# Kernel tuning notes

Hardware: AMD Instinct MI355X
Metric: run time of the kernel (lower is better)

The kernel has to match this reference:

```python
import jax, jax.numpy as jnp
import numpy as np
import math

HIDDEN = 2048
NUM_HEADS = 16
HEAD_DIM = HIDDEN // NUM_HEADS  # 128
B, T = 2, 2048
MAX_POS = 4096
ROPE_BASE = 10000.0


def _rope_cache(dim, max_pos, base):
    inv_freq = 1.0 / (base ** (jnp.arange(0, dim, 2, dtype=jnp.float32) / dim))
    t = jnp.arange(max_pos, dtype=jnp.float32)
    freqs = jnp.einsum('i,j->ij', t, inv_freq)        # [max_pos, dim/2]
    emb = jnp.concatenate([freqs, freqs], axis=-1)     # [max_pos, dim]
    return jnp.cos(emb), jnp.sin(emb)


def setup_inputs() -> dict:
    key = jax.random.key(0)
    ks = jax.random.split(key, 5)
    hidden_states = jax.random.normal(ks[0], (B, T, HIDDEN), dtype=jnp.float32)
    # additive causal mask, large negative (not -inf) for numerical safety
    causal = jnp.triu(jnp.full((T, T), -1e9, dtype=jnp.float32), k=1)
    attention_mask = causal[None, None, :, :]          # [1,1,T,T]
    position_ids = jnp.arange(T, dtype=jnp.int64)
    s = 1.0 / math.sqrt(HIDDEN)
    Wq = jax.random.normal(ks[1], (HIDDEN, HIDDEN), dtype=jnp.float32) * s
    Wk = jax.random.normal(ks[2], (HIDDEN, HIDDEN), dtype=jnp.float32) * s
    Wv = jax.random.normal(ks[3], (HIDDEN, HIDDEN), dtype=jnp.float32) * s
    Wo = jax.random.normal(ks[4], (HIDDEN, HIDDEN), dtype=jnp.float32) * s
    cos_cached, sin_cached = _rope_cache(HEAD_DIM, MAX_POS, ROPE_BASE)
    return {
        'hidden_states': hidden_states,
        'attention_mask': attention_mask,
        'position_ids': position_ids,
        'Wq': Wq, 'Wk': Wk, 'Wv': Wv, 'Wo': Wo,
        'cos_cached': cos_cached, 'sin_cached': sin_cached,
    }


def _apply_rope(x, cos, sin):
    # x: [B, T, nh, hd]; cos/sin: [T, 1, hd] (broadcast over heads)
    x1 = x[..., 0::2]
    x2 = x[..., 1::2]
    x_rot = jnp.stack([-x2, x1], axis=-1).reshape(x.shape)  # interleaved rotate
    return x * cos + x_rot * sin


def reference(hidden_states, attention_mask, position_ids, Wq, Wk, Wv, Wo,
              cos_cached, sin_cached):
    Bs, Ts, H = hidden_states.shape
    nh, hd = NUM_HEADS, HEAD_DIM
    q = (hidden_states @ Wq.T).reshape(Bs, Ts, nh, hd)
    k = (hidden_states @ Wk.T).reshape(Bs, Ts, nh, hd)
    v = (hidden_states @ Wv.T).reshape(Bs, Ts, nh, hd)
    cos = cos_cached[position_ids][:, None, :]  # [T,1,hd]
    sin = sin_cached[position_ids][:, None, :]
    q = _apply_rope(q, cos, sin)
    k = _apply_rope(k, cos, sin)
    # [B, nh, T, hd]
    q = q.transpose(0, 2, 1, 3)
    k = k.transpose(0, 2, 1, 3)
    v = v.transpose(0, 2, 1, 3)
    scores = jnp.einsum('bhqd,bhkd->bhqk', q, k) / math.sqrt(hd)
    scores = scores + attention_mask
    attn = jax.nn.softmax(scores, axis=-1)
    out = jnp.einsum('bhqk,bhkd->bhqd', attn, v)
    out = out.transpose(0, 2, 1, 3).reshape(Bs, Ts, H)
    return out @ Wo.T
```

## Files before the change

kernel.cpp:

```cpp
#include <hip/hip_runtime.h>
#include <cstdint>


typedef __bf16 v8bf __attribute__((ext_vector_type(8)));
typedef float  v4f  __attribute__((ext_vector_type(4)));
typedef float  f32x16 __attribute__((ext_vector_type(16)));

__device__ __forceinline__ uint16_t f2bf(float f) {
  union { float f; uint32_t u; } v; v.f = f;
  uint32_t u = v.u;
  return (uint16_t)((u + 0x7FFFu + ((u >> 16) & 1u)) >> 16);
}

__device__ __forceinline__ uint32_t cvtpk(float lo, float hi) {
  uint32_t w;
  asm("v_cvt_pk_bf16_f32 %0, %1, %2" : "=v"(w) : "v"(lo), "v"(hi));
  return w;
}

__device__ __forceinline__ void gload16(const void* g, void* l) {
  __builtin_amdgcn_global_load_lds(
      (const __attribute__((address_space(1))) void*)g,
      (__attribute__((address_space(3))) void*)l, 16, 0, 0);
}

__global__ void cvt_all_kernel(const float* __restrict__ s0, uint16_t* d0,
                               const float* __restrict__ s1, uint16_t* d1,
                               const float* __restrict__ s2, uint16_t* d2,
                               const float* __restrict__ s3, uint16_t* d3,
                               const float* __restrict__ s4, uint16_t* d4) {
  const float* src; uint16_t* dst; int n4;
  switch (blockIdx.y) {
    case 0: src = s0; dst = d0; n4 = 2097152; break;
    case 1: src = s1; dst = d1; n4 = 1048576; break;
    case 2: src = s2; dst = d2; n4 = 1048576; break;
    case 3: src = s3; dst = d3; n4 = 1048576; break;
    default: src = s4; dst = d4; n4 = 1048576; break;
  }
  int i = blockIdx.x * blockDim.x + threadIdx.x;
  int stride = gridDim.x * blockDim.x;
  for (; i < n4; i += stride) {
    float4 v = reinterpret_cast<const float4*>(src)[i];
    ushort4 o;
    o.x = f2bf(v.x); o.y = f2bf(v.y); o.z = f2bf(v.z); o.w = f2bf(v.w);
    reinterpret_cast<ushort4*>(dst)[i] = o;
  }
}

__device__ __forceinline__ void gemm256_mainloop(
    const uint16_t* __restrict__ A, const uint16_t* __restrict__ Bt,
    int m0, int n0, uint16_t* As, uint16_t* Bs, v4f acc[4][4]) {
  const int tid  = threadIdx.x;
  const int lane = tid & 63, w = tid >> 6;
  const int wm = w >> 1, wn = w & 1;
  const int lrow = lane & 15, lhi = lane >> 4;

  auto stageA = [&](int buf, int k0, int i) {
    int c = i * 512 + tid;
    int row = c >> 3, seg = c & 7;
    int sseg = seg ^ (row & 7);
    gload16(A + (size_t)(m0 + row) * 2048 + k0 + sseg * 8,
            As + buf * 16384 + c * 8);
  };
  auto stageB = [&](int buf, int k0, int i) {
    int c = i * 512 + tid;
    int row = c >> 3, seg = c & 7;
    int sseg = seg ^ (row & 7);
    gload16(Bt + (size_t)(n0 + row) * 2048 + k0 + sseg * 8,
            Bs + buf * 8192 + c * 8);
  };

#pragma unroll
  for (int i = 0; i < 4; ++i) stageA(0, 0, i);
#pragma unroll
  for (int i = 0; i < 2; ++i) stageB(0, 0, i);
#pragma unroll
  for (int i = 0; i < 4; ++i) stageA(1, 64, i);
#pragma unroll
  for (int i = 0; i < 2; ++i) stageB(1, 64, i);
  asm volatile("s_waitcnt vmcnt(6)" ::: "memory");
  __builtin_amdgcn_s_barrier();
  __builtin_amdgcn_sched_barrier(0);

  for (int t = 0; t < 32; ++t) {
    const int cb = t % 3;
    const int sb = (t + 2) % 3;
    const int sk = (t + 2) * 64;
    const uint16_t* Ac = As + cb * 16384;
    const uint16_t* Bc = Bs + cb * 8192;
    const bool do_stage = (t + 2) < 32;
#pragma unroll
    for (int ks = 0; ks < 2; ++ks) {
      v8bf af[4], bfv[4];
#pragma unroll
      for (int mf = 0; mf < 4; ++mf) {
        const int ar = wm * 64 + mf * 16 + lrow;
        const int seg = (ks * 4 + lhi) ^ (ar & 7);
        af[mf] = *reinterpret_cast<const v8bf*>(Ac + ar * 64 + seg * 8);
      }
#pragma unroll
      for (int nf = 0; nf < 4; ++nf) {
        const int br = wn * 64 + nf * 16 + lrow;
        const int seg = (ks * 4 + lhi) ^ (br & 7);
        bfv[nf] = *reinterpret_cast<const v8bf*>(Bc + br * 64 + seg * 8);
      }
      if (do_stage) {
        if (ks == 0) { stageA(sb, sk, 0); stageA(sb, sk, 1); stageB(sb, sk, 0); }
        else         { stageA(sb, sk, 2); stageA(sb, sk, 3); stageB(sb, sk, 1); }
      }
      if (ks == 1) {
        if (t < 30) asm volatile("s_waitcnt vmcnt(6)" ::: "memory");
        else        asm volatile("s_waitcnt vmcnt(0)" ::: "memory");
      } else {
        asm volatile("" ::: "memory");
      }
      __builtin_amdgcn_s_barrier();
      __builtin_amdgcn_sched_barrier(0);
      __builtin_amdgcn_s_setprio(1);
#pragma unroll
      for (int mf = 0; mf < 4; ++mf)
#pragma unroll
        for (int nf = 0; nf < 4; ++nf)
          acc[mf][nf] = __builtin_amdgcn_mfma_f32_16x16x32_bf16(
              af[mf], bfv[nf], acc[mf][nf], 0, 0, 0);
      __builtin_amdgcn_s_setprio(0);
      asm volatile("" ::: "memory");
      __builtin_amdgcn_s_barrier();
      __builtin_amdgcn_sched_barrier(0);
    }
  }
}

__global__ __launch_bounds__(512, 2) void qkv_gemm_kernel(
    const uint16_t* __restrict__ Xbf,
    const uint16_t* __restrict__ Wqb, const uint16_t* __restrict__ Wkb,
    const uint16_t* __restrict__ Wvb,
    const float* __restrict__ cosc, const float* __restrict__ sinc,
    uint16_t* __restrict__ Qh, uint16_t* __restrict__ Kh,
    uint16_t* __restrict__ Vt) {
  __shared__ uint16_t As[3 * 256 * 64];
  __shared__ uint16_t Bs[3 * 128 * 64];
  const int id  = blockIdx.x;
  const int swz = (id & 7) * 96 + (id >> 3);
  const int which = swz >> 8;
  const int rem = swz & 255;
  const int m0 = (rem >> 4) * 256, n0 = (rem & 15) * 128;
  const uint16_t* Wb = (which == 0) ? Wqb : (which == 1) ? Wkb : Wvb;

  v4f acc[4][4];
#pragma unroll
  for (int i = 0; i < 4; ++i)
#pragma unroll
    for (int j = 0; j < 4; ++j) acc[i][j] = (v4f)0.0f;

  gemm256_mainloop(Xbf, Wb, m0, n0, As, Bs, acc);

  const int lane = threadIdx.x & 63;
  const int w = threadIdx.x >> 6, wm = w >> 1, wn = w & 1;
  const int lrow = lane & 15, lhi = lane >> 4;
  const int b = m0 >> 11;

  if (which < 2) {
    uint16_t* dst = (which == 0) ? Qh : Kh;
#pragma unroll
    for (int mf = 0; mf < 4; ++mf) {
#pragma unroll
      for (int nf = 0; nf < 4; ++nf) {
        const int n = n0 + wn * 64 + nf * 16 + lrow;
        const int head = n >> 7, d = n & 127;
#pragma unroll
        for (int r = 0; r < 4; ++r) {
          const int m = m0 + wm * 64 + mf * 16 + lhi * 4 + r;
          const int t = m & 2047;
          float v = acc[mf][nf][r];
          float p = __shfl_xor(v, 1);
          float rot = (n & 1) ? p : -p;
          float cf = cosc[t * 128 + d], sf = sinc[t * 128 + d];
          dst[((size_t)(b * 16 + head) * 2048 + t) * 128 + d] =
              f2bf(v * cf + rot * sf);
        }
      }
    }
  } else {
#pragma unroll
    for (int mf = 0; mf < 4; ++mf) {
#pragma unroll
      for (int nf = 0; nf < 4; ++nf) {
        const int n = n0 + wn * 64 + nf * 16 + lrow;
        const int head = n >> 7, d = n & 127;
        const int m = m0 + wm * 64 + mf * 16 + lhi * 4;
        const int t = m & 2047;
        ushort4 o;
        o.x = f2bf(acc[mf][nf][0]); o.y = f2bf(acc[mf][nf][1]);
        o.z = f2bf(acc[mf][nf][2]); o.w = f2bf(acc[mf][nf][3]);
        *reinterpret_cast<ushort4*>(
            &Vt[((size_t)(b * 16 + head) * 128 + d) * 2048 + t]) = o;
      }
    }
  }
}

__global__ __launch_bounds__(256, 2) void attn_kernel(
    const uint16_t* __restrict__ Qh, const uint16_t* __restrict__ Kh,
    const uint16_t* __restrict__ Vt, uint16_t* __restrict__ Ob) {
  __shared__ uint16_t KV[3][8192];

  const int id = blockIdx.x;
  const int qt = (id < 256) ? (15 - (id >> 5)) : ((id - 256) >> 5);
  const int bh = id & 31;
  const int tid = threadIdx.x, lane = tid & 63, w = tid >> 6;
  const int l31 = lane & 31, hi = lane >> 5;
  const size_t base = (size_t)bh * 2048 * 128;
  const int q0 = qt * 128 + w * 32;
  const int qr = q0 + l31;

  v8bf qf[8];
#pragma unroll
  for (int ks = 0; ks < 8; ++ks)
    qf[ks] = *reinterpret_cast<const v8bf*>(
        Qh + base + (size_t)qr * 128 + ks * 16 + hi * 8);

  f32x16 acc[4];
#pragma unroll
  for (int d = 0; d < 4; ++d) acc[d] = (f32x16)0.0f;
  float m = -1e30f, l = 0.0f;

  auto stage = [&](int buf, int kt) {
    uint16_t* Kd = KV[buf];
    uint16_t* Vd = KV[buf] + 4096;
#pragma unroll
    for (int i = 0; i < 2; ++i) {
      int c = i * 256 + tid;
      int row = c >> 4, seg = c & 15;
      int sseg = seg ^ (row & 7);
      gload16(Kh + base + (size_t)(kt * 32 + row) * 128 + sseg * 8,
              Kd + c * 8);
    }
#pragma unroll
    for (int i = 0; i < 2; ++i) {
      int c = i * 256 + tid;
      int row = c >> 2, seg = c & 3;
      int sseg = seg ^ (row & 3);
      gload16(Vt + base + (size_t)row * 2048 + kt * 32 + sseg * 8,
              Vd + c * 8);
    }
  };

  const float sc = 0.08838834764831845f;
  const int nkt = 4 * (qt + 1);
  stage(0, 0);
  stage(1, 1);
  for (int kt = 0; kt < nkt; ++kt) {
    const int cb = kt % 3;
    if (kt + 1 < nkt) asm volatile("s_waitcnt vmcnt(4)" ::: "memory");
    else              asm volatile("s_waitcnt vmcnt(0)" ::: "memory");
    __builtin_amdgcn_s_barrier();
    __builtin_amdgcn_sched_barrier(0);
    if (kt + 2 < nkt) stage((kt + 2) % 3, kt + 2);

    if (kt * 32 <= q0 + 31) {
      const uint16_t* Kc = KV[cb];
      const uint16_t* Vc = KV[cb] + 4096;
      f32x16 s = (f32x16)0.0f;
      {
        const int swzk = l31 & 7;
#pragma unroll
        for (int ks = 0; ks < 8; ++ks) {
          const int seg = (ks * 2 + hi) ^ swzk;
          v8bf kf = *reinterpret_cast<const v8bf*>(Kc + l31 * 128 + seg * 8);
          s = __builtin_amdgcn_mfma_f32_32x32x16_bf16(kf, qf[ks], s, 0, 0, 0);
        }
      }
      if (kt * 32 + 31 > q0) {
#pragma unroll
        for (int q = 0; q < 4; ++q)
#pragma unroll
          for (int r = 0; r < 4; ++r) {
            const int kc = kt * 32 + q * 8 + hi * 4 + r;
            float v = s[q * 4 + r] * sc;
            s[q * 4 + r] = (kc > qr) ? -1e30f : v;
          }
      } else {
#pragma unroll
        for (int g = 0; g < 16; ++g) s[g] *= sc;
      }
      float t8[8];
#pragma unroll
      for (int g = 0; g < 8; ++g) t8[g] = fmaxf(s[g], s[g + 8]);
      float mx = fmaxf(fmaxf(fmaxf(t8[0], t8[1]), fmaxf(t8[2], t8[3])),
                       fmaxf(fmaxf(t8[4], t8[5]), fmaxf(t8[6], t8[7])));
      mx = fmaxf(mx, __shfl_xor(mx, 32));
      if (!__all(mx - m <= 8.0f)) {
        const float mnew = fmaxf(m, mx);
        const float so = __expf(m - mnew);
        m = mnew;
        l *= so;
#pragma unroll
        for (int d = 0; d < 4; ++d)
#pragma unroll
          for (int g = 0; g < 16; ++g) acc[d][g] *= so;
      }
      float rs = 0.0f;
#pragma unroll
      for (int g = 0; g < 16; ++g) {
        const float pv = __expf(s[g] - m);
        s[g] = pv;
        rs += pv;
      }
      rs += __shfl_xor(rs, 32);
      l += rs;
      union BW { uint32_t w[4]; v8bf v; };
      BW pb[2];
#pragma unroll
      for (int sl = 0; sl < 2; ++sl) {
        uint32_t a0 = cvtpk(s[8 * sl + 0], s[8 * sl + 1]);
        uint32_t a1 = cvtpk(s[8 * sl + 2], s[8 * sl + 3]);
        uint32_t b0 = cvtpk(s[8 * sl + 4], s[8 * sl + 5]);
        uint32_t b1 = cvtpk(s[8 * sl + 6], s[8 * sl + 7]);
        asm("v_permlane32_swap_b32 %0, %1" : "+v"(a0), "+v"(b0));
        asm("v_permlane32_swap_b32 %0, %1" : "+v"(a1), "+v"(b1));
        pb[sl].w[0] = a0; pb[sl].w[1] = a1; pb[sl].w[2] = b0; pb[sl].w[3] = b1;
      }
      const int swzv = l31 & 3;
#pragma unroll
      for (int d = 0; d < 4; ++d) {
        const int row = d * 32 + l31;
#pragma unroll
        for (int sl = 0; sl < 2; ++sl) {
          const int seg = (sl * 2 + hi) ^ swzv;
          v8bf va = *reinterpret_cast<const v8bf*>(Vc + row * 32 + seg * 8);
          acc[d] = __builtin_amdgcn_mfma_f32_32x32x16_bf16(va, pb[sl].v,
                                                           acc[d], 0, 0, 0);
        }
      }
    }
  }

  asm volatile("s_waitcnt vmcnt(0) lgkmcnt(0)" ::: "memory");
  __builtin_amdgcn_s_barrier();
  __builtin_amdgcn_sched_barrier(0);
  uint32_t* L32 = reinterpret_cast<uint32_t*>(&KV[0][0]);
  const float inv = 1.0f / l;
#pragma unroll
  for (int d = 0; d < 4; ++d)
#pragma unroll
    for (int q = 0; q < 4; ++q)
#pragma unroll
      for (int rp = 0; rp < 2; ++rp) {
        const int dd1 = d * 16 + q * 4 + hi * 2 + rp;
        const uint32_t lo16 = f2bf(acc[d][q * 4 + rp * 2] * inv);
        const uint32_t hi16 = f2bf(acc[d][q * 4 + rp * 2 + 1] * inv);
        L32[(w * 32 + l31) * 64 + (dd1 ^ ((l31 & 7) << 3))] =
            lo16 | (hi16 << 16);
      }
  asm volatile("" ::: "memory");
  __builtin_amdgcn_s_barrier();
  __builtin_amdgcn_sched_barrier(0);
  const int b = bh >> 4, head = bh & 15;
  uint32_t* Og = reinterpret_cast<uint32_t*>(Ob);
#pragma unroll
  for (int j = 0; j < 32; ++j) {
    const int qrow = qt * 128 + w * 32 + j;
    const uint32_t v = L32[(w * 32 + j) * 64 + (lane ^ ((j & 7) << 3))];
    Og[((size_t)(b * 2048 + qrow) * 2048 + head * 128) / 2 + lane] = v;
  }
}

__global__ __launch_bounds__(512, 2) void out_gemm_kernel(
    const uint16_t* __restrict__ Abf, const uint16_t* __restrict__ Wob,
    float* __restrict__ out) {
  __shared__ uint16_t As[3 * 256 * 64];
  __shared__ uint16_t Bs[3 * 128 * 64];
  const int id  = blockIdx.x;
  const int swz = (id & 7) * 32 + (id >> 3);
  const int m0 = (swz >> 4) * 256, n0 = (swz & 15) * 128;
  v4f acc[4][4];
#pragma unroll
  for (int i = 0; i < 4; ++i)
#pragma unroll
    for (int j = 0; j < 4; ++j) acc[i][j] = (v4f)0.0f;

  gemm256_mainloop(Abf, Wob, m0, n0, As, Bs, acc);

  const int lane = threadIdx.x & 63;
  const int w = threadIdx.x >> 6, wm = w >> 1, wn = w & 1;
  const int lrow = lane & 15, lhi = lane >> 4;
#pragma unroll
  for (int mf = 0; mf < 4; ++mf)
#pragma unroll
    for (int nf = 0; nf < 4; ++nf) {
      const int n = n0 + wn * 64 + nf * 16 + lrow;
#pragma unroll
      for (int r = 0; r < 4; ++r) {
        const int m = m0 + wm * 64 + mf * 16 + lhi * 4 + r;
        out[(size_t)m * 2048 + n] = acc[mf][nf][r];
      }
    }
}

extern "C" void kernel_launch(void* const* d_in, const int* in_sizes, int n_in,
                              void* d_out, int out_size, void* d_ws,
                              size_t ws_size, hipStream_t stream) {
  const float* hidden = (const float*)d_in[0];
  const float* Wq = (const float*)d_in[3];
  const float* Wk = (const float*)d_in[4];
  const float* Wv = (const float*)d_in[5];
  const float* Wo = (const float*)d_in[6];
  const float* cosc = (const float*)d_in[7];
  const float* sinc = (const float*)d_in[8];
  float* out = (float*)d_out;

  uint16_t* Wqb = (uint16_t*)d_ws;
  uint16_t* Wkb = Wqb + 4194304;
  uint16_t* Wvb = Wkb + 4194304;
  uint16_t* Wob = Wvb + 4194304;
  uint16_t* Xbf = Wob + 4194304;
  uint16_t* Qh  = Xbf + 8388608;
  uint16_t* Kh  = Qh + 8388608;
  uint16_t* Vt  = Kh + 8388608;
  uint16_t* Ob  = Xbf;

  cvt_all_kernel<<<dim3(512, 5), 256, 0, stream>>>(
      hidden, Xbf, Wq, Wqb, Wk, Wkb, Wv, Wvb, Wo, Wob);

  qkv_gemm_kernel<<<dim3(768), 512, 0, stream>>>(
      Xbf, Wqb, Wkb, Wvb, cosc, sinc, Qh, Kh, Vt);

  attn_kernel<<<dim3(512), 256, 0, stream>>>(Qh, Kh, Vt, Ob);

  out_gemm_kernel<<<dim3(256), 512, 0, stream>>>(Ob, Wob, out);
}
```

Baseline: 381.2 us.

## Widen attention KV tile to 64 with double buffering; merge GEMM k-substeps

The attention kernel now processes 64 keys per iteration instead of 32, using two LDS buffers instead of three and a full vmcnt(0) wait before each tile. This halves the number of iterations, barriers and softmax max/rescale passes per query tile, at the cost of less prefetch depth and more registers for the doubled score tiles. The QKV GEMM loop now loads both k-substep fragments up front and runs all MFMAs after a single barrier pair per tile, removing one barrier pair per iteration. That raises register pressure for the fragment arrays.

```diff
diff --git a/kernel.cpp b/kernel.cpp
--- a/kernel.cpp
+++ b/kernel.cpp
@@ -88,46 +88,53 @@
     const int sk = (t + 2) * 64;
     const uint16_t* Ac = As + cb * 16384;
     const uint16_t* Bc = Bs + cb * 8192;
-    const bool do_stage = (t + 2) < 32;
-#pragma unroll
-    for (int ks = 0; ks < 2; ++ks) {
-      v8bf af[4], bfv[4];
-#pragma unroll
-      for (int mf = 0; mf < 4; ++mf) {
-        const int ar = wm * 64 + mf * 16 + lrow;
-        const int seg = (ks * 4 + lhi) ^ (ar & 7);
-        af[mf] = *reinterpret_cast<const v8bf*>(Ac + ar * 64 + seg * 8);
-      }
-#pragma unroll
-      for (int nf = 0; nf < 4; ++nf) {
-        const int br = wn * 64 + nf * 16 + lrow;
-        const int seg = (ks * 4 + lhi) ^ (br & 7);
-        bfv[nf] = *reinterpret_cast<const v8bf*>(Bc + br * 64 + seg * 8);
-      }
-      if (do_stage) {
-        if (ks == 0) { stageA(sb, sk, 0); stageA(sb, sk, 1); stageB(sb, sk, 0); }
-        else         { stageA(sb, sk, 2); stageA(sb, sk, 3); stageB(sb, sk, 1); }
-      }
-      if (ks == 1) {
-        if (t < 30) asm volatile("s_waitcnt vmcnt(6)" ::: "memory");
-        else        asm volatile("s_waitcnt vmcnt(0)" ::: "memory");
-      } else {
-        asm volatile("" ::: "memory");
-      }
-      __builtin_amdgcn_s_barrier();
-      __builtin_amdgcn_sched_barrier(0);
-      __builtin_amdgcn_s_setprio(1);
+    const bool ds = (t + 2) < 32;
+
+    v8bf af[2][4], bfv[2][4];
+#pragma unroll
+    for (int mf = 0; mf < 4; ++mf) {
+      const int ar = wm * 64 + mf * 16 + lrow;
+      af[0][mf] = *reinterpret_cast<const v8bf*>(
+          Ac + ar * 64 + ((lhi ^ (ar & 7)) * 8));
+    }
+#pragma unroll
+    for (int nf = 0; nf < 4; ++nf) {
+      const int br = wn * 64 + nf * 16 + lrow;
+      bfv[0][nf] = *reinterpret_cast<const v8bf*>(
+          Bc + br * 64 + ((lhi ^ (br & 7)) * 8));
+    }
+    if (ds) { stageA(sb, sk, 0); stageA(sb, sk, 1); stageB(sb, sk, 0); }
+#pragma unroll
+    for (int mf = 0; mf < 4; ++mf) {
+      const int ar = wm * 64 + mf * 16 + lrow;
+      af[1][mf] = *reinterpret_cast<const v8bf*>(
+          Ac + ar * 64 + (((4 + lhi) ^ (ar & 7)) * 8));
+    }
+#pragma unroll
+    for (int nf = 0; nf < 4; ++nf) {
+      const int br = wn * 64 + nf * 16 + lrow;
+      bfv[1][nf] = *reinterpret_cast<const v8bf*>(
+          Bc + br * 64 + (((4 + lhi) ^ (br & 7)) * 8));
+    }
+    if (ds) { stageA(sb, sk, 2); stageA(sb, sk, 3); stageB(sb, sk, 1); }
+
+    if (t < 30) asm volatile("s_waitcnt vmcnt(6)" ::: "memory");
+    else        asm volatile("s_waitcnt vmcnt(0)" ::: "memory");
+    __builtin_amdgcn_s_barrier();
+    __builtin_amdgcn_sched_barrier(0);
+    __builtin_amdgcn_s_setprio(1);
+#pragma unroll
+    for (int ks = 0; ks < 2; ++ks)
 #pragma unroll
       for (int mf = 0; mf < 4; ++mf)
 #pragma unroll
         for (int nf = 0; nf < 4; ++nf)
           acc[mf][nf] = __builtin_amdgcn_mfma_f32_16x16x32_bf16(
-              af[mf], bfv[nf], acc[mf][nf], 0, 0, 0);
-      __builtin_amdgcn_s_setprio(0);
-      asm volatile("" ::: "memory");
-      __builtin_amdgcn_s_barrier();
-      __builtin_amdgcn_sched_barrier(0);
-    }
+              af[ks][mf], bfv[ks][nf], acc[mf][nf], 0, 0, 0);
+    __builtin_amdgcn_s_setprio(0);
+    asm volatile("" ::: "memory");
+    __builtin_amdgcn_s_barrier();
+    __builtin_amdgcn_sched_barrier(0);
   }
 }
 
@@ -203,7 +210,8 @@
 __global__ __launch_bounds__(256, 2) void attn_kernel(
     const uint16_t* __restrict__ Qh, const uint16_t* __restrict__ Kh,
     const uint16_t* __restrict__ Vt, uint16_t* __restrict__ Ob) {
-  __shared__ uint16_t KV[3][8192];
+  __shared__ uint16_t Ks[2 * 64 * 128];
+  __shared__ uint16_t Vs[2 * 128 * 64];
 
   const int id = blockIdx.x;
   const int qt = (id < 256) ? (15 - (id >> 5)) : ((id - 256) >> 5);
@@ -226,67 +234,75 @@
   float m = -1e30f, l = 0.0f;
 
   auto stage = [&](int buf, int kt) {
-    uint16_t* Kd = KV[buf];
-    uint16_t* Vd = KV[buf] + 4096;
-#pragma unroll
-    for (int i = 0; i < 2; ++i) {
+    uint16_t* Kd = Ks + buf * 8192;
+    uint16_t* Vd = Vs + buf * 8192;
+#pragma unroll
+    for (int i = 0; i < 4; ++i) {
       int c = i * 256 + tid;
       int row = c >> 4, seg = c & 15;
+      int sseg = seg ^ (row & 15);
+      gload16(Kh + base + (size_t)(kt * 64 + row) * 128 + sseg * 8,
+              Kd + c * 8);
+    }
+#pragma unroll
+    for (int i = 0; i < 4; ++i) {
+      int c = i * 256 + tid;
+      int row = c >> 3, seg = c & 7;
       int sseg = seg ^ (row & 7);
-      gload16(Kh + base + (size_t)(kt * 32 + row) * 128 + sseg * 8,
-              Kd + c * 8);
-    }
-#pragma unroll
-    for (int i = 0; i < 2; ++i) {
-      int c = i * 256 + tid;
-      int row = c >> 2, seg = c & 3;
-      int sseg = seg ^ (row & 3);
-      gload16(Vt + base + (size_t)row * 2048 + kt * 32 + sseg * 8,
+      gload16(Vt + base + (size_t)row * 2048 + kt * 64 + sseg * 8,
               Vd + c * 8);
     }
   };
 
   const float sc = 0.08838834764831845f;
-  const int nkt = 4 * (qt + 1);
+  const int nkt = 2 * (qt + 1);
   stage(0, 0);
-  stage(1, 1);
   for (int kt = 0; kt < nkt; ++kt) {
-    const int cb = kt % 3;
-    if (kt + 1 < nkt) asm volatile("s_waitcnt vmcnt(4)" ::: "memory");
-    else              asm volatile("s_waitcnt vmcnt(0)" ::: "memory");
+    const int cur = kt & 1;
+    asm volatile("s_waitcnt vmcnt(0)" ::: "memory");
     __builtin_amdgcn_s_barrier();
     __builtin_amdgcn_sched_barrier(0);
-    if (kt + 2 < nkt) stage((kt + 2) % 3, kt + 2);
-
-    if (kt * 32 <= q0 + 31) {
-      const uint16_t* Kc = KV[cb];
-      const uint16_t* Vc = KV[cb] + 4096;
-      f32x16 s = (f32x16)0.0f;
-      {
-        const int swzk = l31 & 7;
+    if (kt + 1 < nkt) stage(cur ^ 1, kt + 1);
+    const uint16_t* Kc = Ks + cur * 8192;
+    const uint16_t* Vc = Vs + cur * 8192;
+
+    if (kt * 64 <= q0 + 31) {
+      f32x16 s[2];
+      s[0] = (f32x16)0.0f; s[1] = (f32x16)0.0f;
+#pragma unroll
+      for (int kb = 0; kb < 2; ++kb) {
+        const int row = kb * 32 + l31;
+        const int swzk = row & 15;
 #pragma unroll
         for (int ks = 0; ks < 8; ++ks) {
           const int seg = (ks * 2 + hi) ^ swzk;
-          v8bf kf = *reinterpret_cast<const v8bf*>(Kc + l31 * 128 + seg * 8);
-          s = __builtin_amdgcn_mfma_f32_32x32x16_bf16(kf, qf[ks], s, 0, 0, 0);
+          v8bf kf = *reinterpret_cast<const v8bf*>(Kc + row * 128 + seg * 8);
+          s[kb] = __builtin_amdgcn_mfma_f32_32x32x16_bf16(kf, qf[ks], s[kb],
+                                                          0, 0, 0);
         }
       }
-      if (kt * 32 + 31 > q0) {
-#pragma unroll
-        for (int q = 0; q < 4; ++q)
-#pragma unroll
-          for (int r = 0; r < 4; ++r) {
-            const int kc = kt * 32 + q * 8 + hi * 4 + r;
-            float v = s[q * 4 + r] * sc;
-            s[q * 4 + r] = (kc > qr) ? -1e30f : v;
-          }
+      if (kt * 64 + 63 > q0) {
+#pragma unroll
+        for (int kb = 0; kb < 2; ++kb)
+#pragma unroll
+          for (int q = 0; q < 4; ++q)
+#pragma unroll
+            for (int r = 0; r < 4; ++r) {
+              const int kc = kt * 64 + kb * 32 + q * 8 + hi * 4 + r;
+              float v = s[kb][q * 4 + r] * sc;
+              s[kb][q * 4 + r] = (kc > qr) ? -1e30f : v;
+            }
       } else {
 #pragma unroll
-        for (int g = 0; g < 16; ++g) s[g] *= sc;
+        for (int kb = 0; kb < 2; ++kb)
+#pragma unroll
+          for (int g = 0; g < 16; ++g) s[kb][g] *= sc;
       }
       float t8[8];
 #pragma unroll
-      for (int g = 0; g < 8; ++g) t8[g] = fmaxf(s[g], s[g + 8]);
+      for (int g = 0; g < 8; ++g)
+        t8[g] = fmaxf(fmaxf(s[0][g], s[0][g + 8]),
+                      fmaxf(s[1][g], s[1][g + 8]));
       float mx = fmaxf(fmaxf(fmaxf(t8[0], t8[1]), fmaxf(t8[2], t8[3])),
                        fmaxf(fmaxf(t8[4], t8[5]), fmaxf(t8[6], t8[7])));
       mx = fmaxf(mx, __shfl_xor(mx, 32));
@@ -302,34 +318,39 @@
       }
       float rs = 0.0f;
 #pragma unroll
-      for (int g = 0; g < 16; ++g) {
-        const float pv = __expf(s[g] - m);
-        s[g] = pv;
-        rs += pv;
-      }
+      for (int kb = 0; kb < 2; ++kb)
+#pragma unroll
+        for (int g = 0; g < 16; ++g) {
+          const float pv = __expf(s[kb][g] - m);
+          s[kb][g] = pv;
+          rs += pv;
+        }
       rs += __shfl_xor(rs, 32);
       l += rs;
       union BW { uint32_t w[4]; v8bf v; };
-      BW pb[2];
-#pragma unroll
-      for (int sl = 0; sl < 2; ++sl) {
-        uint32_t a0 = cvtpk(s[8 * sl + 0], s[8 * sl + 1]);
-        uint32_t a1 = cvtpk(s[8 * sl + 2], s[8 * sl + 3]);
-        uint32_t b0 = cvtpk(s[8 * sl + 4], s[8 * sl + 5]);
-        uint32_t b1 = cvtpk(s[8 * sl + 6], s[8 * sl + 7]);
-        asm("v_permlane32_swap_b32 %0, %1" : "+v"(a0), "+v"(b0));
-        asm("v_permlane32_swap_b32 %0, %1" : "+v"(a1), "+v"(b1));
-        pb[sl].w[0] = a0; pb[sl].w[1] = a1; pb[sl].w[2] = b0; pb[sl].w[3] = b1;
-      }
-      const int swzv = l31 & 3;
+      BW pb[4];
+#pragma unroll
+      for (int kb = 0; kb < 2; ++kb)
+#pragma unroll
+        for (int sl = 0; sl < 2; ++sl) {
+          uint32_t a0 = cvtpk(s[kb][8 * sl + 0], s[kb][8 * sl + 1]);
+          uint32_t a1 = cvtpk(s[kb][8 * sl + 2], s[kb][8 * sl + 3]);
+          uint32_t b0 = cvtpk(s[kb][8 * sl + 4], s[kb][8 * sl + 5]);
+          uint32_t b1 = cvtpk(s[kb][8 * sl + 6], s[kb][8 * sl + 7]);
+          asm("v_permlane32_swap_b32 %0, %1" : "+v"(a0), "+v"(b0));
+          asm("v_permlane32_swap_b32 %0, %1" : "+v"(a1), "+v"(b1));
+          BW& f = pb[kb * 2 + sl];
+          f.w[0] = a0; f.w[1] = a1; f.w[2] = b0; f.w[3] = b1;
+        }
 #pragma unroll
       for (int d = 0; d < 4; ++d) {
         const int row = d * 32 + l31;
-#pragma unroll
-        for (int sl = 0; sl < 2; ++sl) {
-          const int seg = (sl * 2 + hi) ^ swzv;
-          v8bf va = *reinterpret_cast<const v8bf*>(Vc + row * 32 + seg * 8);
-          acc[d] = __builtin_amdgcn_mfma_f32_32x32x16_bf16(va, pb[sl].v,
+        const int swzv = row & 7;
+#pragma unroll
+        for (int sl4 = 0; sl4 < 4; ++sl4) {
+          const int seg = (sl4 * 2 + hi) ^ swzv;
+          v8bf va = *reinterpret_cast<const v8bf*>(Vc + row * 64 + seg * 8);
+          acc[d] = __builtin_amdgcn_mfma_f32_32x32x16_bf16(va, pb[sl4].v,
                                                            acc[d], 0, 0, 0);
         }
       }
@@ -339,7 +360,7 @@
   asm volatile("s_waitcnt vmcnt(0) lgkmcnt(0)" ::: "memory");
   __builtin_amdgcn_s_barrier();
   __builtin_amdgcn_sched_barrier(0);
-  uint32_t* L32 = reinterpret_cast<uint32_t*>(&KV[0][0]);
+  uint32_t* L32 = reinterpret_cast<uint32_t*>(&Ks[0]);
   const float inv = 1.0f / l;
 #pragma unroll
   for (int d = 0; d < 4; ++d)
```

Measured after the change: 394.3 us. 1.03x slower.
